# Optimization experiments

Hardware: AMD Instinct MI355X
Metric: run time of the kernel (lower is better)

Reference implementation:

```python
import jax, jax.numpy as jnp
import numpy as np
from jax import lax

PATCH = 9
DILATION = 1
EPS = 1e-6


def _l2norm(x):
    # L2-normalize over channel dim (dim=1), eps added to sum of squares before sqrt
    norm = jnp.sqrt(jnp.sum(x * x, axis=1, keepdims=True) + EPS)
    return x / norm


def setup_inputs() -> dict:
    key = jax.random.key(0)
    k1, k2 = jax.random.split(key)
    feature1 = jax.random.normal(k1, (4, 64, 64, 64), dtype=jnp.float32)
    feature2 = jax.random.normal(k2, (4, 64, 64, 64), dtype=jnp.float32)
    return {"feature1": feature1, "feature2": feature2}


def _correlation(f1, f2, patch, dilation):
    # SpatialCorrelationSampler with ks=1, stride=1, pad=0:
    # corr[b, pi, pj, y, x] = sum_c f1[b,c,y,x] * f2[b,c,y+dy,x+dx]
    # dy = (pi - patch//2)*dilation, dx = (pj - patch//2)*dilation; OOB = 0.
    b, c, h, w = f1.shape
    half = (patch // 2) * dilation
    f2p = jnp.pad(f2, ((0, 0), (0, 0), (half, half), (half, half)))
    d = jnp.arange(patch, dtype=jnp.int32) * dilation  # offsets into padded map
    offs = jnp.stack(jnp.meshgrid(d, d, indexing="ij"), axis=-1).reshape(-1, 2)  # [P^2, 2]

    def one_disp(off):
        f2s = lax.dynamic_slice(f2p, (0, 0, off[0], off[1]), (b, c, h, w))
        return jnp.sum(f1 * f2s, axis=1)  # [b, h, w]

    corr = lax.map(one_disp, offs)  # [P^2, b, h, w] (sequential -> low peak memory)
    return jnp.transpose(corr, (1, 0, 2, 3))  # [b, P^2, h, w]


def reference(feature1, feature2):
    f1 = _l2norm(feature1)
    f2 = _l2norm(feature2)
    b, c, h, w = f1.shape
    corr = _correlation(f1, f2, PATCH, DILATION)  # [b, P^2, h, w]
    corr = corr.reshape(b, PATCH * PATCH, h * w)
    return jax.nn.relu(corr)
```

## Files before the change

kernel.cpp:

```cpp
#include <hip/hip_runtime.h>

#define BB 4
#define CC 64
#define C2 32
#define HH 64
#define WW 64
#define PATCH 9
#define HALF 4
#define P2 81
#define HW 4096
#define IMG (CC * HW)

typedef _Float16 v2h __attribute__((ext_vector_type(2)));

static __device__ __forceinline__ unsigned pk(float a, float b) {
    v2h h = {(_Float16)a, (_Float16)b};
    return __builtin_bit_cast(unsigned, h);
}

__global__ __launch_bounds__(64) void corr_kernel(const float* __restrict__ f1,
                                                  const float* __restrict__ f2,
                                                  float* __restrict__ out) {
    __shared__ unsigned sB[C2 * 72];
    __shared__ float sS2[64];

    const int x   = threadIdx.x;
    const int bid = blockIdx.x;
    const int xcd = bid & 7;
    const int s   = bid >> 3;
    const int b   = s / 72;
    const int r   = s - b * 72;
    const int yo  = r / 9;
    const int dy  = r - yo * 9;
    const int y   = xcd * 8 + yo;
    const int y2  = y + dy - HALF;

    float* ob = out + b * (P2 * HW) + y * WW + x;

    if ((unsigned)y2 >= HH) {
#pragma unroll
        for (int dx = 0; dx < PATCH; ++dx)
            ob[(dy * PATCH + dx) * HW] = 0.f;
        return;
    }

    const float* f1r = f1 + b * IMG + y * WW + x;
    unsigned a[C2];
    float ssq1 = 0.f;
#pragma unroll
    for (int c2 = 0; c2 < C2; ++c2) {
        float u0 = f1r[(2 * c2) * HW];
        float u1 = f1r[(2 * c2 + 1) * HW];
        ssq1 = fmaf(u0, u0, fmaf(u1, u1, ssq1));
        a[c2] = pk(u0, u1);
    }

    const float* f2r = f2 + b * IMG + y2 * WW;
#pragma unroll
    for (int it = 0; it < 8; ++it) {
        int item = x + it * 64;
        int c2 = item >> 4, k = item & 15;
        const float* p = f2r + 4 * k;
        float4 va = *(const float4*)(p + (2 * c2) * HW);
        float4 vb = *(const float4*)(p + (2 * c2 + 1) * HW);
        uint4 u = {pk(va.x, vb.x), pk(va.y, vb.y), pk(va.z, vb.z), pk(va.w, vb.w)};
        *(uint4*)&sB[c2 * 72 + 4 + 4 * k] = u;
    }
#pragma unroll
    for (int it = 0; it < 4; ++it) {
        int j = x + it * 64;
        int c2 = j >> 3, e = j & 7;
        sB[c2 * 72 + (e < 4 ? e : 64 + e)] = 0u;
    }
    __syncthreads();

    float acc[PATCH];
#pragma unroll
    for (int i = 0; i < PATCH; ++i) acc[i] = 0.f;
    float ssq2 = 0.f;
#pragma unroll
    for (int c2 = 0; c2 < C2; ++c2) {
        v2h a2 = __builtin_bit_cast(v2h, a[c2]);
        const unsigned* br = &sB[c2 * 72 + x];
#pragma unroll
        for (int dx = 0; dx < PATCH; ++dx)
            acc[dx] = __builtin_amdgcn_fdot2(a2, __builtin_bit_cast(v2h, br[dx]),
                                             acc[dx], false);
        v2h c4 = __builtin_bit_cast(v2h, br[4]);
        ssq2 = __builtin_amdgcn_fdot2(c4, c4, ssq2, false);
    }
    sS2[x] = rsqrtf(ssq2 + 1e-6f);
    __syncthreads();

    const float s1 = rsqrtf(ssq1 + 1e-6f);
#pragma unroll
    for (int dx = 0; dx < PATCH; ++dx) {
        int col = x + dx - HALF;
        col = min(max(col, 0), WW - 1);
        ob[(dy * PATCH + dx) * HW] = fmaxf(acc[dx] * s1 * sS2[col], 0.f);
    }
}

extern "C" void kernel_launch(void* const* d_in, const int* in_sizes, int n_in,
                              void* d_out, int out_size, void* d_ws, size_t ws_size,
                              hipStream_t stream) {
    const float* f1 = (const float*)d_in[0];
    const float* f2 = (const float*)d_in[1];
    float* out = (float*)d_out;
    (void)d_ws; (void)ws_size;

    corr_kernel<<<BB * HH * PATCH, 64, 0, stream>>>(f1, f2, out);
}
```

Measured before the change: 66.05 us.

## Split channels across wave halves with two-column register blocking per thread

Each thread now computes two adjacent output columns over half of the channels. The two halves of the wave are combined with cross-lane shuffles. Shared-memory reads of f2 become 64-bit vector loads that are reused across both columns, which cuts LDS load count per dot product, and f1 loads become float2. The cost is more accumulator registers, the shuffle reduction, and output stores with interleaved column mapping that may coalesce less cleanly.

New measurement: 65.86 us. Within noise of the previous version (-0.3%).

```diff
diff --git a/kernel.cpp b/kernel.cpp
--- a/kernel.cpp
+++ b/kernel.cpp
@@ -17,6 +17,9 @@
     v2h h = {(_Float16)a, (_Float16)b};
     return __builtin_bit_cast(unsigned, h);
 }
+static __device__ __forceinline__ v2h bch(unsigned u) {
+    return __builtin_bit_cast(v2h, u);
+}
 
 __global__ __launch_bounds__(64) void corr_kernel(const float* __restrict__ f1,
                                                   const float* __restrict__ f2,
@@ -24,7 +27,9 @@
     __shared__ unsigned sB[C2 * 72];
     __shared__ float sS2[64];
 
-    const int x   = threadIdx.x;
+    const int tid = threadIdx.x;
+    const int m   = tid & 31;
+    const int h   = tid >> 5;
     const int bid = blockIdx.x;
     const int xcd = bid & 7;
     const int s   = bid >> 3;
@@ -35,7 +40,8 @@
     const int y   = xcd * 8 + yo;
     const int y2  = y + dy - HALF;
 
-    float* ob = out + b * (P2 * HW) + y * WW + x;
+    const int xx = 2 * m + h;
+    float* ob = out + b * (P2 * HW) + y * WW + xx;
 
     if ((unsigned)y2 >= HH) {
 #pragma unroll
@@ -44,21 +50,24 @@
         return;
     }
 
-    const float* f1r = f1 + b * IMG + y * WW + x;
-    unsigned a[C2];
-    float ssq1 = 0.f;
+    const float* f1r = f1 + b * IMG + y * WW + 2 * m;
+    unsigned a0[16], a1[16];
+    float ssq1_0 = 0.f, ssq1_1 = 0.f;
 #pragma unroll
-    for (int c2 = 0; c2 < C2; ++c2) {
-        float u0 = f1r[(2 * c2) * HW];
-        float u1 = f1r[(2 * c2 + 1) * HW];
-        ssq1 = fmaf(u0, u0, fmaf(u1, u1, ssq1));
-        a[c2] = pk(u0, u1);
+    for (int i = 0; i < 16; ++i) {
+        const int c = 32 * h + 2 * i;
+        float2 va = *(const float2*)(f1r + c * HW);
+        float2 vb = *(const float2*)(f1r + (c + 1) * HW);
+        ssq1_0 = fmaf(va.x, va.x, fmaf(vb.x, vb.x, ssq1_0));
+        ssq1_1 = fmaf(va.y, va.y, fmaf(vb.y, vb.y, ssq1_1));
+        a0[i] = pk(va.x, vb.x);
+        a1[i] = pk(va.y, vb.y);
     }
 
     const float* f2r = f2 + b * IMG + y2 * WW;
 #pragma unroll
     for (int it = 0; it < 8; ++it) {
-        int item = x + it * 64;
+        int item = tid + it * 64;
         int c2 = item >> 4, k = item & 15;
         const float* p = f2r + 4 * k;
         float4 va = *(const float4*)(p + (2 * c2) * HW);
@@ -68,36 +77,56 @@
     }
 #pragma unroll
     for (int it = 0; it < 4; ++it) {
-        int j = x + it * 64;
+        int j = tid + it * 64;
         int c2 = j >> 3, e = j & 7;
         sB[c2 * 72 + (e < 4 ? e : 64 + e)] = 0u;
     }
     __syncthreads();
 
-    float acc[PATCH];
+    float acc0[PATCH], acc1[PATCH];
 #pragma unroll
-    for (int i = 0; i < PATCH; ++i) acc[i] = 0.f;
-    float ssq2 = 0.f;
+    for (int i = 0; i < PATCH; ++i) { acc0[i] = 0.f; acc1[i] = 0.f; }
+    float ssq2_0 = 0.f, ssq2_1 = 0.f;
 #pragma unroll
-    for (int c2 = 0; c2 < C2; ++c2) {
-        v2h a2 = __builtin_bit_cast(v2h, a[c2]);
-        const unsigned* br = &sB[c2 * 72 + x];
+    for (int i = 0; i < 16; ++i) {
+        const unsigned* br = &sB[(16 * h + i) * 72 + 2 * m];
+        uint2 p0 = *(const uint2*)(br + 0);
+        uint2 p1 = *(const uint2*)(br + 2);
+        uint2 p2 = *(const uint2*)(br + 4);
+        uint2 p3 = *(const uint2*)(br + 6);
+        uint2 p4 = *(const uint2*)(br + 8);
+        v2h w[10] = {bch(p0.x), bch(p0.y), bch(p1.x), bch(p1.y), bch(p2.x),
+                     bch(p2.y), bch(p3.x), bch(p3.y), bch(p4.x), bch(p4.y)};
+        v2h A0 = bch(a0[i]), A1 = bch(a1[i]);
 #pragma unroll
-        for (int dx = 0; dx < PATCH; ++dx)
-            acc[dx] = __builtin_amdgcn_fdot2(a2, __builtin_bit_cast(v2h, br[dx]),
-                                             acc[dx], false);
-        v2h c4 = __builtin_bit_cast(v2h, br[4]);
-        ssq2 = __builtin_amdgcn_fdot2(c4, c4, ssq2, false);
+        for (int dx = 0; dx < PATCH; ++dx) {
+            acc0[dx] = __builtin_amdgcn_fdot2(A0, w[dx],     acc0[dx], false);
+            acc1[dx] = __builtin_amdgcn_fdot2(A1, w[dx + 1], acc1[dx], false);
+        }
+        ssq2_0 = __builtin_amdgcn_fdot2(w[4], w[4], ssq2_0, false);
+        ssq2_1 = __builtin_amdgcn_fdot2(w[5], w[5], ssq2_1, false);
     }
-    sS2[x] = rsqrtf(ssq2 + 1e-6f);
+
+#pragma unroll
+    for (int dx = 0; dx < PATCH; ++dx) {
+        acc0[dx] += __shfl_xor(acc0[dx], 32);
+        acc1[dx] += __shfl_xor(acc1[dx], 32);
+    }
+    ssq1_0 += __shfl_xor(ssq1_0, 32);
+    ssq1_1 += __shfl_xor(ssq1_1, 32);
+    ssq2_0 += __shfl_xor(ssq2_0, 32);
+    ssq2_1 += __shfl_xor(ssq2_1, 32);
+
+    sS2[xx] = rsqrtf((h ? ssq2_1 : ssq2_0) + 1e-6f);
     __syncthreads();
 
-    const float s1 = rsqrtf(ssq1 + 1e-6f);
+    const float s1 = rsqrtf((h ? ssq1_1 : ssq1_0) + 1e-6f);
 #pragma unroll
     for (int dx = 0; dx < PATCH; ++dx) {
-        int col = x + dx - HALF;
+        float av = h ? acc1[dx] : acc0[dx];
+        int col = xx + dx - HALF;
         col = min(max(col, 0), WW - 1);
-        ob[(dy * PATCH + dx) * HW] = fmaxf(acc[dx] * s1 * sS2[col], 0.f);
+        ob[(dy * PATCH + dx) * HW] = fmaxf(av * s1 * sS2[col], 0.f);
     }
 }
 
```
